# Optimization experiments

Hardware: AMD Instinct MI355X
Metric: run time of the kernel (lower is better)

The kernel has to match this reference:

```python
import math
import jax, jax.numpy as jnp
import numpy as np

B, T, D = 2, 2048, 1024
NH = 16
HD = D // NH


def setup_inputs() -> dict:
    key = jax.random.key(0)
    k1, k2, k3 = jax.random.split(key, 3)
    s = 0.02
    return {
        "x": jax.random.normal(k1, (B, T, D), dtype=jnp.float32),
        "w_qkv": jax.random.normal(k2, (D, 3 * D), dtype=jnp.float32) * s,
        "w_proj": jax.random.normal(k3, (D, D), dtype=jnp.float32) * s,
    }


def reference(x, w_qkv, w_proj):
    b, t, c = x.shape
    qkv = x @ w_qkv  # [B,T,3D]
    q, k, v = jnp.split(qkv, 3, axis=-1)
    # [B,NH,T,HD]
    q = q.reshape(b, t, NH, HD).transpose(0, 2, 1, 3)
    k = k.reshape(b, t, NH, HD).transpose(0, 2, 1, 3)
    v = v.reshape(b, t, NH, HD).transpose(0, 2, 1, 3)
    scores = jnp.einsum("bhqd,bhkd->bhqk", q, k) / math.sqrt(HD)
    mask = jnp.tril(jnp.ones((t, t), dtype=x.dtype))  # [T,T]
    # faithful to source: scaled scores are multiplied by the mask, then -1e9 added where masked
    masked = scores * mask + (1.0 - mask) * (-1e9)
    a = jax.nn.softmax(masked, axis=-1)
    out = jnp.einsum("bhqk,bhkd->bhqd", a, v)  # [B,NH,T,HD]
    out = out.transpose(0, 2, 1, 3).reshape(b, t, c)
    return out @ w_proj
```

## Files before the change

### kernel.cpp

```cpp
#include <hip/hip_runtime.h>
#include <stdint.h>

#define B_SZ 2
#define T_SEQ 2048
#define D_MODEL 1024
#define NHEADS 16
#define HDIM 64
#define QKV_P (3 * D_MODEL)

typedef unsigned short u16;
typedef uint32_t u32;
typedef __attribute__((ext_vector_type(4))) float f32x4;
typedef __attribute__((ext_vector_type(8))) short s16x8;
typedef __attribute__((ext_vector_type(4))) short s16x4;

__device__ __forceinline__ u16 f2bf(float f) {
  union { float f; uint32_t u; } v; v.f = f;
  uint32_t r = v.u + 0x7fffu + ((v.u >> 16) & 1u);
  return (u16)(r >> 16);
}

__device__ __forceinline__ float fastexp2(float x) {
  float r;
  asm volatile("v_exp_f32 %0, %1" : "=v"(r) : "v"(x));
  return r;
}

__device__ __forceinline__ u32 cvtpk(float lo, float hi) {
  u32 r;
  asm volatile("v_cvt_pk_bf16_f32 %0, %1, %2" : "=v"(r) : "v"(lo), "v"(hi));
  return r;
}

__device__ __forceinline__ void async16(const void* g, void* l) {
  __builtin_amdgcn_global_load_lds((const __attribute__((address_space(1))) void*)g,
                                   (__attribute__((address_space(3))) void*)l,
                                   16, 0, 0);
}

__global__ __launch_bounds__(256) void prep(const float* __restrict__ x,
                                            const float* __restrict__ wq,
                                            const float* __restrict__ wp,
                                            u16* __restrict__ xb,
                                            u16* __restrict__ wqkvT,
                                            u16* __restrict__ wprojT) {
  const int bid = blockIdx.x, tid = threadIdx.x;
  if (bid < 4096) {
    int i = bid * 256 + tid;
    float4 v = ((const float4*)x)[i];
    ushort4 o;
    o.x = f2bf(v.x); o.y = f2bf(v.y); o.z = f2bf(v.z); o.w = f2bf(v.w);
    ((ushort4*)xb)[i] = o;
    return;
  }
  __shared__ float tile[32][33];
  const float* in; u16* outp; int C, bx, by;
  if (bid < 4096 + 3072) {
    int bb = bid - 4096; in = wq; outp = wqkvT; C = 3072; bx = bb % 96; by = bb / 96;
  } else {
    int bb = bid - 7168; in = wp; outp = wprojT; C = 1024; bx = bb % 32; by = bb / 32;
  }
  const int tx = tid & 31, ty = tid >> 5;
  const int c0 = bx * 32, r0 = by * 32;
#pragma unroll
  for (int i = 0; i < 4; i++)
    tile[ty + i * 8][tx] = in[(size_t)(r0 + ty + i * 8) * C + c0 + tx];
  __syncthreads();
#pragma unroll
  for (int i = 0; i < 4; i++)
    outp[(size_t)(c0 + ty + i * 8) * D_MODEL + r0 + tx] = f2bf(tile[tx][ty + i * 8]);
}

template <int F32OUT, int VFUSE>
__global__ __launch_bounds__(256) void gemm_bt(const u16* __restrict__ A,
                                               const u16* __restrict__ BT,
                                               void* __restrict__ Cout,
                                               u16* __restrict__ vTout,
                                               int M, int N, int K) {
  __shared__ u16 As[2][128 * 32];
  __shared__ u16 Bs[2][128 * 32];
  const int tid = threadIdx.x;
  const int lane = tid & 63, w = tid >> 6;
  const int l15 = lane & 15, g = lane >> 4;
  const int wr = w >> 1, wc = w & 1;
  const int bn = blockIdx.x, bm = blockIdx.y;
  const u16* Ab = A + (size_t)bm * 128 * K;
  const u16* Bb = BT + (size_t)bn * 128 * K;
  f32x4 acc[4][4];
#pragma unroll
  for (int i = 0; i < 4; i++)
#pragma unroll
    for (int j = 0; j < 4; j++) acc[i][j] = (f32x4){0.f, 0.f, 0.f, 0.f};
  const int c0 = tid, c1 = tid + 256;

#define GSTAGE(buf, kt_)                                                          \
  do {                                                                            \
    async16(Ab + (size_t)(c0 >> 2) * K + (kt_) + (c0 & 3) * 8, (char*)As[buf] + c0 * 16); \
    async16(Ab + (size_t)(c1 >> 2) * K + (kt_) + (c1 & 3) * 8, (char*)As[buf] + c1 * 16); \
    async16(Bb + (size_t)(c0 >> 2) * K + (kt_) + (c0 & 3) * 8, (char*)Bs[buf] + c0 * 16); \
    async16(Bb + (size_t)(c1 >> 2) * K + (kt_) + (c1 & 3) * 8, (char*)Bs[buf] + c1 * 16); \
  } while (0)

  GSTAGE(0, 0);
  int cur = 0;
  for (int kt = 0; kt < K; kt += 32) {
    if (kt + 32 < K) {
      GSTAGE(cur ^ 1, kt + 32);
      asm volatile("s_waitcnt vmcnt(4)" ::: "memory");
    } else {
      asm volatile("s_waitcnt vmcnt(0)" ::: "memory");
    }
    __syncthreads();
    s16x8 af[4], bfr[4];
#pragma unroll
    for (int i = 0; i < 4; i++)
      af[i] = *(const s16x8*)(As[cur] + (wr * 64 + i * 16 + l15) * 32 + g * 8);
#pragma unroll
    for (int j = 0; j < 4; j++)
      bfr[j] = *(const s16x8*)(Bs[cur] + (wc * 64 + j * 16 + l15) * 32 + g * 8);
#pragma unroll
    for (int i = 0; i < 4; i++)
#pragma unroll
      for (int j = 0; j < 4; j++)
        acc[i][j] = __builtin_amdgcn_mfma_f32_16x16x32_bf16(af[i], bfr[j], acc[i][j], 0, 0, 0);
    __syncthreads();
    cur ^= 1;
  }

  if (VFUSE && bn >= 16) {
    const int bloc = bm >> 4;
    const int tb = bm * 128 + wr * 64 - bloc * T_SEQ;
#pragma unroll
    for (int i = 0; i < 4; i++) {
      const int tl = tb + i * 16 + g * 4;
#pragma unroll
      for (int j = 0; j < 4; j++) {
        const int hh = bn * 128 + wc * 64 + j * 16 + l15 - 2048;
        uint2 pk;
        pk.x = cvtpk(acc[i][j][0], acc[i][j][1]);
        pk.y = cvtpk(acc[i][j][2], acc[i][j][3]);
        *(uint2*)&vTout[(size_t)(bloc * 1024 + hh) * T_SEQ + tl] = pk;
      }
    }
    return;
  }
#pragma unroll
  for (int i = 0; i < 4; i++) {
    const int row0 = bm * 128 + wr * 64 + i * 16 + g * 4;
#pragma unroll
    for (int j = 0; j < 4; j++) {
      const int col = bn * 128 + wc * 64 + j * 16 + l15;
#pragma unroll
      for (int r = 0; r < 4; r++) {
        if (F32OUT)
          ((float*)Cout)[(size_t)(row0 + r) * N + col] = acc[i][j][r];
        else
          ((u16*)Cout)[(size_t)(row0 + r) * N + col] = f2bf(acc[i][j][r]);
      }
    }
  }
}

__global__ __launch_bounds__(256, 4) void flash_attn(const u16* __restrict__ qkv,
                                                     const u16* __restrict__ vT,
                                                     u16* __restrict__ attn) {
  __shared__ u16 Ks[2][64 * 64];
  __shared__ u16 Vs[2][64 * 64];
  const int tid = threadIdx.x;
  const int lane = tid & 63, w = tid >> 6;
  const int l15 = lane & 15, g = lane >> 4;
  const int id = blockIdx.x;
  const int bh = ((id & 7) << 2) | ((id >> 3) & 3);
  const int j = (id >> 5) & 7, k4 = (id >> 8) & 3;
  const int qs = (k4 == 0) ? (31 - j) : (k4 == 1) ? (16 + j) : (k4 == 2) ? (15 - j) : j;
  const int b = bh >> 4, h = bh & 15;

  const size_t qrow = (size_t)(b * T_SEQ + qs * 64 + w * 16 + l15);
  s16x8 qf[2];
  qf[0] = *(const s16x8*)(qkv + qrow * QKV_P + h * HDIM + 0 * 32 + g * 8);
  qf[1] = *(const s16x8*)(qkv + qrow * QKV_P + h * HDIM + 1 * 32 + g * 8);

  f32x4 O[4];
#pragma unroll
  for (int t = 0; t < 4; t++) O[t] = (f32x4){0.f, 0.f, 0.f, 0.f};
  float m_s = -1e30f, l_s = 0.f;
  const int qrl = w * 16 + l15;
  const float sc = 0.18033688011112042f;

#define STAGE(buf, kvt_)                                                                     \
  do {                                                                                       \
    _Pragma("unroll") for (int i_ = 0; i_ < 2; i_++) {                                       \
      int o_ = (tid + i_ * 256) * 16;                                                        \
      int lo_ = o_ ^ (((o_ >> 7) & 7) << 4);                                                 \
      int row_ = lo_ >> 7;                                                                   \
      int byt_ = lo_ & 127;                                                                  \
      async16(qkv + (size_t)(b * T_SEQ + (kvt_) * 64 + row_) * QKV_P + D_MODEL + h * HDIM +  \
                  (byt_ >> 1),                                                               \
              (char*)Ks[buf] + o_);                                                          \
      async16(vT + (size_t)(bh * HDIM + row_) * T_SEQ + (kvt_) * 64 + (byt_ >> 1),           \
              (char*)Vs[buf] + o_);                                                          \
    }                                                                                        \
  } while (0)

  STAGE(0, 0);
  int cur = 0;
  const int nt = qs + 1;
  for (int kvt = 0; kvt < nt; ++kvt) {
    if (kvt < qs) {
      STAGE(cur ^ 1, kvt + 1);
      asm volatile("s_waitcnt vmcnt(4)" ::: "memory");
    } else {
      asm volatile("s_waitcnt vmcnt(0)" ::: "memory");
    }
    __syncthreads();

    f32x4 S[4];
#pragma unroll
    for (int t16 = 0; t16 < 4; t16++) S[t16] = (f32x4){0.f, 0.f, 0.f, 0.f};
#pragma unroll
    for (int t16 = 0; t16 < 4; t16++)
#pragma unroll
      for (int kk = 0; kk < 2; kk++) {
        int key = t16 * 16 + l15;
        int bp = (key * 128 + kk * 64 + g * 16) ^ ((key & 7) << 4);
        s16x8 kf = *(const s16x8*)((const char*)Ks[cur] + bp);
        S[t16] = __builtin_amdgcn_mfma_f32_16x16x32_bf16(kf, qf[kk], S[t16], 0, 0, 0);
      }

    if (kvt == qs) {
#pragma unroll
      for (int t16 = 0; t16 < 4; t16++)
#pragma unroll
        for (int r = 0; r < 4; r++)
          if (t16 * 16 + g * 4 + r > qrl) S[t16][r] = -3e38f;
    }
    float mx = fmaxf(fmaxf(fmaxf(S[0][0], S[0][1]), fmaxf(S[0][2], S[0][3])),
                     fmaxf(fmaxf(S[1][0], S[1][1]), fmaxf(S[1][2], S[1][3])));
    mx = fmaxf(mx, fmaxf(fmaxf(fmaxf(S[2][0], S[2][1]), fmaxf(S[2][2], S[2][3])),
                         fmaxf(fmaxf(S[3][0], S[3][1]), fmaxf(S[3][2], S[3][3]))));
    mx = fmaxf(mx, __shfl_xor(mx, 16));
    mx = fmaxf(mx, __shfl_xor(mx, 32));
    if (!__all(mx - m_s <= 40.f)) {
      const float mnew = fmaxf(m_s, mx);
      const float alpha = fastexp2((m_s - mnew) * sc);
      m_s = mnew;
      l_s *= alpha;
#pragma unroll
      for (int t = 0; t < 4; t++)
#pragma unroll
        for (int r = 0; r < 4; r++) O[t][r] *= alpha;
    }
    const float msc = m_s * sc;
    float p[16];
#pragma unroll
    for (int t16 = 0; t16 < 4; t16++)
#pragma unroll
      for (int r = 0; r < 4; r++) p[t16 * 4 + r] = fastexp2(fmaf(S[t16][r], sc, -msc));
    float ps = 0.f;
#pragma unroll
    for (int i = 0; i < 16; i++) ps += p[i];
    ps += __shfl_xor(ps, 16);
    ps += __shfl_xor(ps, 32);
    l_s += ps;

#pragma unroll
    for (int t16 = 0; t16 < 4; t16++) {
      union { u32 u[2]; s16x4 v; } pbv;
      pbv.u[0] = cvtpk(p[t16 * 4 + 0], p[t16 * 4 + 1]);
      pbv.u[1] = cvtpk(p[t16 * 4 + 2], p[t16 * 4 + 3]);
#pragma unroll
      for (int t = 0; t < 4; t++) {
        int hd = t * 16 + l15;
        int bp = (hd * 128 + t16 * 32 + g * 8) ^ ((hd & 7) << 4);
        s16x4 vf = *(const s16x4*)((const char*)Vs[cur] + bp);
        O[t] = __builtin_amdgcn_mfma_f32_16x16x16bf16_1k(vf, pbv.v, O[t], 0, 0, 0);
      }
    }
    __syncthreads();
    cur ^= 1;
  }

  const float inv = 1.0f / l_s;
  const size_t row = (size_t)(b * T_SEQ + qs * 64 + w * 16 + l15);
#pragma unroll
  for (int t = 0; t < 4; t++)
#pragma unroll
    for (int pr = 0; pr < 2; pr++) {
      u32 pk = cvtpk(O[t][pr * 2 + 0] * inv, O[t][pr * 2 + 1] * inv);
      *(u32*)&attn[row * D_MODEL + h * HDIM + t * 16 + g * 4 + pr * 2] = pk;
    }
}

extern "C" void kernel_launch(void* const* d_in, const int* in_sizes, int n_in,
                              void* d_out, int out_size, void* d_ws, size_t ws_size,
                              hipStream_t stream) {
  const float* x = (const float*)d_in[0];
  const float* w_qkv = (const float*)d_in[1];
  const float* w_proj = (const float*)d_in[2];
  float* out = (float*)d_out;
  char* ws = (char*)d_ws;
  const size_t MB = (size_t)1 << 20;
  if (ws_size < 56 * MB) return;
  u16* xb = (u16*)(ws + 0);
  u16* wqkvT = (u16*)(ws + 8 * MB);
  u16* wprojT = (u16*)(ws + 14 * MB);
  u16* qkv = (u16*)(ws + 16 * MB);
  u16* vT = (u16*)(ws + 40 * MB);
  u16* attn = (u16*)(ws + 48 * MB);

  prep<<<8192, 256, 0, stream>>>(x, w_qkv, w_proj, xb, wqkvT, wprojT);
  gemm_bt<0, 1><<<dim3(QKV_P / 128, (B_SZ * T_SEQ) / 128), 256, 0, stream>>>(
      xb, wqkvT, qkv, vT, B_SZ * T_SEQ, QKV_P, D_MODEL);
  flash_attn<<<1024, 256, 0, stream>>>(qkv, vT, attn);
  gemm_bt<1, 0><<<dim3(D_MODEL / 128, (B_SZ * T_SEQ) / 128), 256, 0, stream>>>(
      attn, wprojT, out, nullptr, B_SZ * T_SEQ, D_MODEL, D_MODEL);
}
```

Baseline: 114.2 us.

## Rework GEMMs with 64-wide K tiles, swizzled LDS, XCD-aware grid; MFMA row sums in attention

The GEMM kernel now stages 64-wide K tiles into XOR-swizzled LDS, hardcodes K, remaps a 1D grid so neighbouring blocks share A rows per XCD, raises MFMA priority, and replaces __syncthreads with raw barriers. The goal is fewer loop iterations and barriers, fewer LDS bank conflicts and better L2 reuse. In flash attention, the softmax row sum is computed by an MFMA against a ones vector instead of a per-lane sum plus shuffles. The max shuffle reduction now runs only when a rescale is needed. The MFMA row sum adds matrix work and sums bf16-rounded probabilities, and the raw barriers rely on explicit waitcnt for correctness.

```diff
diff --git a/kernel.cpp b/kernel.cpp
--- a/kernel.cpp
+++ b/kernel.cpp
@@ -36,6 +36,11 @@
   __builtin_amdgcn_global_load_lds((const __attribute__((address_space(1))) void*)g,
                                    (__attribute__((address_space(3))) void*)l,
                                    16, 0, 0);
+}
+
+__device__ __forceinline__ void rawbar() {
+  __builtin_amdgcn_s_barrier();
+  __builtin_amdgcn_sched_barrier(0);
 }
 
 __global__ __launch_bounds__(256) void prep(const float* __restrict__ x,
@@ -71,19 +76,23 @@
     outp[(size_t)(c0 + ty + i * 8) * D_MODEL + r0 + tx] = f2bf(tile[tx][ty + i * 8]);
 }
 
-template <int F32OUT, int VFUSE>
-__global__ __launch_bounds__(256) void gemm_bt(const u16* __restrict__ A,
-                                               const u16* __restrict__ BT,
-                                               void* __restrict__ Cout,
-                                               u16* __restrict__ vTout,
-                                               int M, int N, int K) {
-  __shared__ u16 As[2][128 * 32];
-  __shared__ u16 Bs[2][128 * 32];
+template <int F32OUT, int VFUSE, int NBN>
+__global__ __launch_bounds__(256, 2) void gemm128(const u16* __restrict__ A,
+                                                  const u16* __restrict__ BT,
+                                                  void* __restrict__ Cout,
+                                                  u16* __restrict__ vTout,
+                                                  int N) {
+  __shared__ u16 As[2][128 * 64];
+  __shared__ u16 Bs[2][128 * 64];
   const int tid = threadIdx.x;
   const int lane = tid & 63, w = tid >> 6;
   const int l15 = lane & 15, g = lane >> 4;
   const int wr = w >> 1, wc = w & 1;
-  const int bn = blockIdx.x, bm = blockIdx.y;
+  const int id = blockIdx.x;
+  const int cid = id >> 3;
+  const int bm = (id & 7) * 4 + cid / NBN;
+  const int bn = cid % NBN;
+  const int K = 1024;
   const u16* Ab = A + (size_t)bm * 128 * K;
   const u16* Bb = BT + (size_t)bn * 128 * K;
   f32x4 acc[4][4];
@@ -91,54 +100,71 @@
   for (int i = 0; i < 4; i++)
 #pragma unroll
     for (int j = 0; j < 4; j++) acc[i][j] = (f32x4){0.f, 0.f, 0.f, 0.f};
-  const int c0 = tid, c1 = tid + 256;
-
-#define GSTAGE(buf, kt_)                                                          \
-  do {                                                                            \
-    async16(Ab + (size_t)(c0 >> 2) * K + (kt_) + (c0 & 3) * 8, (char*)As[buf] + c0 * 16); \
-    async16(Ab + (size_t)(c1 >> 2) * K + (kt_) + (c1 & 3) * 8, (char*)As[buf] + c1 * 16); \
-    async16(Bb + (size_t)(c0 >> 2) * K + (kt_) + (c0 & 3) * 8, (char*)Bs[buf] + c0 * 16); \
-    async16(Bb + (size_t)(c1 >> 2) * K + (kt_) + (c1 & 3) * 8, (char*)Bs[buf] + c1 * 16); \
+
+#define G1_LD(dst, srcb, kt_)                                                \
+  do {                                                                       \
+    _Pragma("unroll") for (int i_ = 0; i_ < 4; i_++) {                       \
+      int o_ = (tid + i_ * 256) * 16;                                        \
+      int lo_ = o_ ^ (((o_ >> 7) & 7) << 4);                                 \
+      async16((srcb) + (size_t)(lo_ >> 7) * K + (kt_) + ((lo_ & 127) >> 1),  \
+              (char*)(dst) + o_);                                            \
+    }                                                                        \
   } while (0)
 
-  GSTAGE(0, 0);
+  G1_LD(As[0], Ab, 0);
+  G1_LD(Bs[0], Bb, 0);
   int cur = 0;
-  for (int kt = 0; kt < K; kt += 32) {
-    if (kt + 32 < K) {
-      GSTAGE(cur ^ 1, kt + 32);
-      asm volatile("s_waitcnt vmcnt(4)" ::: "memory");
+  for (int t = 0; t < 16; t++) {
+    if (t < 15) {
+      G1_LD(As[cur ^ 1], Ab, (t + 1) * 64);
+      G1_LD(Bs[cur ^ 1], Bb, (t + 1) * 64);
+      asm volatile("s_waitcnt vmcnt(8)" ::: "memory");
     } else {
       asm volatile("s_waitcnt vmcnt(0)" ::: "memory");
     }
-    __syncthreads();
-    s16x8 af[4], bfr[4];
+    rawbar();
+    s16x8 af[4][2], bf[4][2];
+#pragma unroll
+    for (int i = 0; i < 4; i++) {
+      int r_ = wr * 64 + i * 16 + l15;
+#pragma unroll
+      for (int kk = 0; kk < 2; kk++)
+        af[i][kk] = *(const s16x8*)((const char*)As[cur] +
+                                    ((r_ * 128 + kk * 64 + g * 16) ^ ((r_ & 7) << 4)));
+    }
+#pragma unroll
+    for (int jn = 0; jn < 4; jn++) {
+      int n_ = wc * 64 + jn * 16 + l15;
+#pragma unroll
+      for (int kk = 0; kk < 2; kk++)
+        bf[jn][kk] = *(const s16x8*)((const char*)Bs[cur] +
+                                     ((n_ * 128 + kk * 64 + g * 16) ^ ((n_ & 7) << 4)));
+    }
+    __builtin_amdgcn_s_setprio(1);
 #pragma unroll
     for (int i = 0; i < 4; i++)
-      af[i] = *(const s16x8*)(As[cur] + (wr * 64 + i * 16 + l15) * 32 + g * 8);
-#pragma unroll
-    for (int j = 0; j < 4; j++)
-      bfr[j] = *(const s16x8*)(Bs[cur] + (wc * 64 + j * 16 + l15) * 32 + g * 8);
-#pragma unroll
-    for (int i = 0; i < 4; i++)
-#pragma unroll
-      for (int j = 0; j < 4; j++)
-        acc[i][j] = __builtin_amdgcn_mfma_f32_16x16x32_bf16(af[i], bfr[j], acc[i][j], 0, 0, 0);
-    __syncthreads();
+#pragma unroll
+      for (int jn = 0; jn < 4; jn++) {
+        acc[i][jn] = __builtin_amdgcn_mfma_f32_16x16x32_bf16(af[i][0], bf[jn][0], acc[i][jn], 0, 0, 0);
+        acc[i][jn] = __builtin_amdgcn_mfma_f32_16x16x32_bf16(af[i][1], bf[jn][1], acc[i][jn], 0, 0, 0);
+      }
+    __builtin_amdgcn_s_setprio(0);
+    rawbar();
     cur ^= 1;
   }
 
   if (VFUSE && bn >= 16) {
-    const int bloc = bm >> 4;
-    const int tb = bm * 128 + wr * 64 - bloc * T_SEQ;
 #pragma unroll
     for (int i = 0; i < 4; i++) {
-      const int tl = tb + i * 16 + g * 4;
-#pragma unroll
-      for (int j = 0; j < 4; j++) {
-        const int hh = bn * 128 + wc * 64 + j * 16 + l15 - 2048;
+      const int m = bm * 128 + wr * 64 + i * 16 + g * 4;
+      const int bloc = m >> 11;
+      const int tl = m & 2047;
+#pragma unroll
+      for (int jn = 0; jn < 4; jn++) {
+        const int hh = bn * 128 + wc * 64 + jn * 16 + l15 - 2048;
         uint2 pk;
-        pk.x = cvtpk(acc[i][j][0], acc[i][j][1]);
-        pk.y = cvtpk(acc[i][j][2], acc[i][j][3]);
+        pk.x = cvtpk(acc[i][jn][0], acc[i][jn][1]);
+        pk.y = cvtpk(acc[i][jn][2], acc[i][jn][3]);
         *(uint2*)&vTout[(size_t)(bloc * 1024 + hh) * T_SEQ + tl] = pk;
       }
     }
@@ -148,14 +174,14 @@
   for (int i = 0; i < 4; i++) {
     const int row0 = bm * 128 + wr * 64 + i * 16 + g * 4;
 #pragma unroll
-    for (int j = 0; j < 4; j++) {
-      const int col = bn * 128 + wc * 64 + j * 16 + l15;
+    for (int jn = 0; jn < 4; jn++) {
+      const int col = bn * 128 + wc * 64 + jn * 16 + l15;
 #pragma unroll
       for (int r = 0; r < 4; r++) {
         if (F32OUT)
-          ((float*)Cout)[(size_t)(row0 + r) * N + col] = acc[i][j][r];
+          ((float*)Cout)[(size_t)(row0 + r) * N + col] = acc[i][jn][r];
         else
-          ((u16*)Cout)[(size_t)(row0 + r) * N + col] = f2bf(acc[i][j][r]);
+          ((u16*)Cout)[(size_t)(row0 + r) * N + col] = f2bf(acc[i][jn][r]);
       }
     }
   }
@@ -183,9 +209,11 @@
   f32x4 O[4];
 #pragma unroll
   for (int t = 0; t < 4; t++) O[t] = (f32x4){0.f, 0.f, 0.f, 0.f};
-  float m_s = -1e30f, l_s = 0.f;
+  f32x4 sumacc = (f32x4){0.f, 0.f, 0.f, 0.f};
+  float m_s = -1e30f;
   const int qrl = w * 16 + l15;
   const float sc = 0.18033688011112042f;
+  const s16x4 onesf = {(short)0x3F80, (short)0x3F80, (short)0x3F80, (short)0x3F80};
 
 #define STAGE(buf, kvt_)                                                                     \
   do {                                                                                       \
@@ -212,7 +240,7 @@
     } else {
       asm volatile("s_waitcnt vmcnt(0)" ::: "memory");
     }
-    __syncthreads();
+    rawbar();
 
     f32x4 S[4];
 #pragma unroll
@@ -234,17 +262,17 @@
         for (int r = 0; r < 4; r++)
           if (t16 * 16 + g * 4 + r > qrl) S[t16][r] = -3e38f;
     }
-    float mx = fmaxf(fmaxf(fmaxf(S[0][0], S[0][1]), fmaxf(S[0][2], S[0][3])),
-                     fmaxf(fmaxf(S[1][0], S[1][1]), fmaxf(S[1][2], S[1][3])));
-    mx = fmaxf(mx, fmaxf(fmaxf(fmaxf(S[2][0], S[2][1]), fmaxf(S[2][2], S[2][3])),
-                         fmaxf(fmaxf(S[3][0], S[3][1]), fmaxf(S[3][2], S[3][3]))));
-    mx = fmaxf(mx, __shfl_xor(mx, 16));
-    mx = fmaxf(mx, __shfl_xor(mx, 32));
-    if (!__all(mx - m_s <= 40.f)) {
+    float pmx = fmaxf(fmaxf(fmaxf(S[0][0], S[0][1]), fmaxf(S[0][2], S[0][3])),
+                      fmaxf(fmaxf(S[1][0], S[1][1]), fmaxf(S[1][2], S[1][3])));
+    pmx = fmaxf(pmx, fmaxf(fmaxf(fmaxf(S[2][0], S[2][1]), fmaxf(S[2][2], S[2][3])),
+                           fmaxf(fmaxf(S[3][0], S[3][1]), fmaxf(S[3][2], S[3][3]))));
+    if (!__all(pmx - m_s <= 40.f)) {
+      float mx = fmaxf(pmx, __shfl_xor(pmx, 16));
+      mx = fmaxf(mx, __shfl_xor(mx, 32));
       const float mnew = fmaxf(m_s, mx);
       const float alpha = fastexp2((m_s - mnew) * sc);
       m_s = mnew;
-      l_s *= alpha;
+      sumacc[0] *= alpha; sumacc[1] *= alpha; sumacc[2] *= alpha; sumacc[3] *= alpha;
 #pragma unroll
       for (int t = 0; t < 4; t++)
 #pragma unroll
@@ -256,18 +284,13 @@
     for (int t16 = 0; t16 < 4; t16++)
 #pragma unroll
       for (int r = 0; r < 4; r++) p[t16 * 4 + r] = fastexp2(fmaf(S[t16][r], sc, -msc));
-    float ps = 0.f;
-#pragma unroll
-    for (int i = 0; i < 16; i++) ps += p[i];
-    ps += __shfl_xor(ps, 16);
-    ps += __shfl_xor(ps, 32);
-    l_s += ps;
 
 #pragma unroll
     for (int t16 = 0; t16 < 4; t16++) {
       union { u32 u[2]; s16x4 v; } pbv;
       pbv.u[0] = cvtpk(p[t16 * 4 + 0], p[t16 * 4 + 1]);
       pbv.u[1] = cvtpk(p[t16 * 4 + 2], p[t16 * 4 + 3]);
+      sumacc = __builtin_amdgcn_mfma_f32_16x16x16bf16_1k(onesf, pbv.v, sumacc, 0, 0, 0);
 #pragma unroll
       for (int t = 0; t < 4; t++) {
         int hd = t * 16 + l15;
@@ -276,11 +299,11 @@
         O[t] = __builtin_amdgcn_mfma_f32_16x16x16bf16_1k(vf, pbv.v, O[t], 0, 0, 0);
       }
     }
-    __syncthreads();
+    rawbar();
     cur ^= 1;
   }
 
-  const float inv = 1.0f / l_s;
+  const float inv = 1.0f / sumacc[0];
   const size_t row = (size_t)(b * T_SEQ + qs * 64 + w * 16 + l15);
 #pragma unroll
   for (int t = 0; t < 4; t++)
@@ -309,9 +332,7 @@
   u16* attn = (u16*)(ws + 48 * MB);
 
   prep<<<8192, 256, 0, stream>>>(x, w_qkv, w_proj, xb, wqkvT, wprojT);
-  gemm_bt<0, 1><<<dim3(QKV_P / 128, (B_SZ * T_SEQ) / 128), 256, 0, stream>>>(
-      xb, wqkvT, qkv, vT, B_SZ * T_SEQ, QKV_P, D_MODEL);
+  gemm128<0, 1, 24><<<768, 256, 0, stream>>>(xb, wqkvT, qkv, vT, QKV_P);
   flash_attn<<<1024, 256, 0, stream>>>(qkv, vT, attn);
-  gemm_bt<1, 0><<<dim3(D_MODEL / 128, (B_SZ * T_SEQ) / 128), 256, 0, stream>>>(
-      attn, wprojT, out, nullptr, B_SZ * T_SEQ, D_MODEL, D_MODEL);
-}
+  gemm128<1, 0, 8><<<256, 256, 0, stream>>>(attn, wprojT, out, nullptr, D_MODEL);
+}
```

Result: faster. 108.3 us (-5.2%).
